# Optimization experiments

Measured on AMD Instinct MI355X. Metric: run time of the kernel, lower is better.

Reference implementation:

```python
import jax, jax.numpy as jnp
import numpy as np

B = 16
N_IN_PER = 256
N_SKIP_PER = 1024
C_IN = 256
C_SKIP = 128


def setup_inputs() -> dict:
    key = jax.random.key(0)
    ks = jax.random.split(key, 8)
    n_in = B * N_IN_PER
    n_skip = B * N_SKIP_PER
    in_x = jax.random.normal(ks[0], (n_in, C_IN), dtype=jnp.float32)
    in_pos = jax.random.uniform(ks[1], (n_in, 3), dtype=jnp.float32)
    in_batch = jnp.repeat(jnp.arange(B, dtype=jnp.int64), N_IN_PER)
    skip_x = jax.random.normal(ks[2], (n_skip, C_SKIP), dtype=jnp.float32)
    skip_pos = jax.random.uniform(ks[3], (n_skip, 3), dtype=jnp.float32)
    skip_batch = jnp.repeat(jnp.arange(B, dtype=jnp.int64), N_SKIP_PER)
    d_cat = C_IN + C_SKIP + 3  # 387
    W1 = jax.random.normal(ks[4], (d_cat, 256), dtype=jnp.float32) * (1.0 / np.sqrt(d_cat))
    b1 = jnp.zeros((256,), dtype=jnp.float32)
    W2 = jax.random.normal(ks[5], (256, 256), dtype=jnp.float32) * (1.0 / 16.0)
    b2 = jnp.zeros((256,), dtype=jnp.float32)
    return {"in_x": in_x, "in_pos": in_pos, "in_batch": in_batch,
            "skip_x": skip_x, "skip_pos": skip_pos, "skip_batch": skip_batch,
            "W1": W1, "b1": b1, "W2": W2, "b2": b2, "knn_num": 3}


def _knn_interpolate(in_x, in_pos, in_batch, skip_pos, skip_batch, k):
    # Pairwise squared distances fine->coarse, masked across graphs. [Ns, Ni]
    d2 = jnp.sum((skip_pos[:, None, :] - in_pos[None, :, :]) ** 2, axis=-1)
    cross = skip_batch[:, None] != in_batch[None, :]
    d2 = jnp.where(cross, jnp.inf, d2)
    _, idx = jax.lax.top_k(-d2, k)  # [Ns, k] nearest coarse neighbors
    nb_pos = in_pos[idx]  # [Ns, k, 3]
    dist = jnp.sqrt(jnp.sum((nb_pos - skip_pos[:, None, :]) ** 2, axis=-1))
    dist = jnp.maximum(dist, 1e-10)
    w = 1.0 / dist
    w = w / (jnp.sum(w, axis=-1, keepdims=True) + 1e-16)  # per-target normalization
    return jnp.einsum('nk,nkc->nc', w, in_x[idx])  # [Ns, C_in]


def reference(in_x, in_pos, in_batch, skip_x, skip_pos, skip_batch, W1, b1, W2, b2, knn_num):
    interp = _knn_interpolate(in_x, in_pos, in_batch, skip_pos, skip_batch, knn_num)
    h = jnp.concatenate([interp, skip_x, skip_pos], axis=1)  # [Ns, 387]
    h = jax.nn.relu(h @ W1 + b1)
    h = jax.nn.relu(h @ W2 + b2)
    return h
```

## Files before the change

kernel.cpp:

```cpp
#include <hip/hip_runtime.h>
#include <hip/hip_bf16.h>


typedef __bf16 bf16x8 __attribute__((ext_vector_type(8)));
typedef float  f32x4  __attribute__((ext_vector_type(4)));

__device__ __forceinline__ unsigned short f2bf(float f) {
  __hip_bfloat16 h = __float2bfloat16(f);
  return __builtin_bit_cast(unsigned short, h);
}

#define GLDS16(G, L)                                                          \
  __builtin_amdgcn_global_load_lds(                                           \
      (const __attribute__((address_space(1))) void*)(G),                     \
      (__attribute__((address_space(3))) void*)(L), 16, 0, 0)

static constexpr int MROWS  = 16384;
static constexpr int KPAD   = 416;
static constexpr int KREAL  = 387;

__global__ __launch_bounds__(256) void prep_weights(
    const float* __restrict__ W1, const float* __restrict__ W2,
    unsigned short* __restrict__ W1t, unsigned short* __restrict__ W2t)
{
  const int k = blockIdx.x;
  const int n = threadIdx.x;
  {
    float v = (k < KREAL) ? W1[(size_t)k * 256 + n] : 0.f;
    W1t[(size_t)n * KPAD + k] = f2bf(v);
  }
  if (k < 256) {
    W2t[(size_t)n * 256 + k] = f2bf(W2[(size_t)k * 256 + n]);
  }
}

__global__ __launch_bounds__(256) void knn_build_h(
    const float* __restrict__ in_x,
    const float* __restrict__ in_pos,
    const float* __restrict__ skip_x,
    const float* __restrict__ skip_pos,
    unsigned short* __restrict__ H)
{
  __shared__ float P[3][256];
  const int tid = threadIdx.x;
  const int s0  = blockIdx.x << 2;
  const int ib  = (s0 >> 10) << 8;
  {
    const float* bp = in_pos + (size_t)ib * 3;
    for (int i = tid; i < 768; i += 256) P[i % 3][i / 3] = bp[i];
  }
  __syncthreads();

  const int wid = tid >> 6, lane = tid & 63;
  const int s = s0 + wid;
  const float sx = skip_pos[(size_t)s * 3 + 0];
  const float sy = skip_pos[(size_t)s * 3 + 1];
  const float sz = skip_pos[(size_t)s * 3 + 2];

  float d2[4];
#pragma unroll
  for (int q = 0; q < 4; ++q) {
    const int i = lane + (q << 6);
    const float dx = __fsub_rn(sx, P[0][i]);
    const float dy = __fsub_rn(sy, P[1][i]);
    const float dz = __fsub_rn(sz, P[2][i]);
    d2[q] = __fadd_rn(__fadd_rn(__fmul_rn(dx, dx), __fmul_rn(dy, dy)),
                      __fmul_rn(dz, dz));
  }

  int   gsel[3];
  float wsel[3];
  float wsum = 0.f;
#pragma unroll
  for (int p = 0; p < 3; ++p) {
    float bd = d2[0];
    int   bi = lane;
#pragma unroll
    for (int q = 1; q < 4; ++q) {
      const int i = lane + (q << 6);
      if (d2[q] < bd) { bd = d2[q]; bi = i; }
    }
#pragma unroll
    for (int m = 1; m < 64; m <<= 1) {
      const float od = __shfl_xor(bd, m);
      const int   oi = __shfl_xor(bi, m);
      if (od < bd || (od == bd && oi < bi)) { bd = od; bi = oi; }
    }
    if ((bi & 63) == lane) d2[bi >> 6] = 3.4e38f;
    gsel[p] = bi;
    const float dx = __fsub_rn(P[0][bi], sx);
    const float dy = __fsub_rn(P[1][bi], sy);
    const float dz = __fsub_rn(P[2][bi], sz);
    float dist = sqrtf(__fadd_rn(__fadd_rn(__fmul_rn(dx, dx), __fmul_rn(dy, dy)),
                                 __fmul_rn(dz, dz)));
    dist = fmaxf(dist, 1e-10f);
    const float w = 1.0f / dist;
    wsel[p] = w;
    wsum += w;
  }
  const float denom = wsum + 1e-16f;
  const float w0 = wsel[0] / denom;
  const float w1 = wsel[1] / denom;
  const float w2 = wsel[2] / denom;

  const f32x4* x0 = (const f32x4*)(in_x + (size_t)(ib + gsel[0]) * 256);
  const f32x4* x1 = (const f32x4*)(in_x + (size_t)(ib + gsel[1]) * 256);
  const f32x4* x2 = (const f32x4*)(in_x + (size_t)(ib + gsel[2]) * 256);
  const f32x4 a = x0[lane], b = x1[lane], c = x2[lane];

  unsigned short* hr = H + (size_t)s * KPAD;
  ushort4 o4;
  o4.x = f2bf(w0 * a.x + w1 * b.x + w2 * c.x);
  o4.y = f2bf(w0 * a.y + w1 * b.y + w2 * c.y);
  o4.z = f2bf(w0 * a.z + w1 * b.z + w2 * c.z);
  o4.w = f2bf(w0 * a.w + w1 * b.w + w2 * c.w);
  *(ushort4*)(hr + (lane << 2)) = o4;

  const float2 sv = ((const float2*)(skip_x + (size_t)s * 128))[lane];
  ushort2 o2;
  o2.x = f2bf(sv.x);
  o2.y = f2bf(sv.y);
  *(ushort2*)(hr + 256 + (lane << 1)) = o2;

  if (lane < 32) {
    float v = (lane == 0) ? sx : (lane == 1) ? sy : (lane == 2) ? sz : 0.f;
    hr[384 + lane] = f2bf(v);
  }
}

template <int K, bool OUT_BF16>
__global__ __launch_bounds__(256) void gemm_bt_relu(
    const unsigned short* __restrict__ A,
    const unsigned short* __restrict__ Bt,
    const float* __restrict__ bias,
    void* __restrict__ Out)
{
  __shared__ unsigned short As[128 * 32];
  __shared__ unsigned short Bs[128 * 32];
  const int tid = threadIdx.x, lane = tid & 63, wid = tid >> 6;
  const int m0 = blockIdx.x << 7, n0 = blockIdx.y << 7;

  const int srow = tid >> 2;
  const int scol = (tid & 3) << 3;
  const unsigned short* gA0 = A + (size_t)(m0 + srow) * K + scol;
  const unsigned short* gA1 = gA0 + (size_t)64 * K;
  const unsigned short* gB0 = Bt + (size_t)(n0 + srow) * K + scol;
  const unsigned short* gB1 = gB0 + (size_t)64 * K;
  unsigned short* lA0 = As + wid * 512;
  unsigned short* lA1 = As + 2048 + wid * 512;
  unsigned short* lB0 = Bs + wid * 512;
  unsigned short* lB1 = Bs + 2048 + wid * 512;

  const int wr = (wid >> 1) << 6;
  const int wc = (wid & 1) << 6;
  const int fr = lane & 15;
  const int ko = (lane >> 4) << 3;

  f32x4 acc[4][4] = {};

  for (int ks = 0; ks < K / 32; ++ks) {
    const int k0 = ks << 5;
    GLDS16(gA0 + k0, lA0);
    GLDS16(gA1 + k0, lA1);
    GLDS16(gB0 + k0, lB0);
    GLDS16(gB1 + k0, lB1);
    __syncthreads();
    bf16x8 af[4], bf[4];
#pragma unroll
    for (int m = 0; m < 4; ++m)
      af[m] = *(const bf16x8*)&As[(wr + m * 16 + fr) * 32 + ko];
#pragma unroll
    for (int n = 0; n < 4; ++n)
      bf[n] = *(const bf16x8*)&Bs[(wc + n * 16 + fr) * 32 + ko];
#pragma unroll
    for (int m = 0; m < 4; ++m)
#pragma unroll
      for (int n = 0; n < 4; ++n)
        acc[m][n] =
            __builtin_amdgcn_mfma_f32_16x16x32_bf16(af[m], bf[n], acc[m][n], 0, 0, 0);
    __syncthreads();
  }

  const int r0 = m0 + wr + ((lane >> 4) << 2);
  const int c0 = n0 + wc + fr;
  float bn[4];
#pragma unroll
  for (int n = 0; n < 4; ++n) bn[n] = bias[c0 + n * 16];
#pragma unroll
  for (int m = 0; m < 4; ++m) {
#pragma unroll
    for (int j = 0; j < 4; ++j) {
      const size_t row = (size_t)(r0 + m * 16 + j);
#pragma unroll
      for (int n = 0; n < 4; ++n) {
        const float v = fmaxf(acc[m][n][j] + bn[n], 0.f);
        if constexpr (OUT_BF16)
          ((unsigned short*)Out)[row * 256 + c0 + n * 16] = f2bf(v);
        else
          ((float*)Out)[row * 256 + c0 + n * 16] = v;
      }
    }
  }
}

extern "C" void kernel_launch(void* const* d_in, const int* in_sizes, int n_in,
                              void* d_out, int out_size, void* d_ws, size_t ws_size,
                              hipStream_t stream) {
  const float* in_x     = (const float*)d_in[0];
  const float* in_pos   = (const float*)d_in[1];
  const float* skip_x   = (const float*)d_in[3];
  const float* skip_pos = (const float*)d_in[4];
  const float* W1       = (const float*)d_in[6];
  const float* bias1    = (const float*)d_in[7];
  const float* W2       = (const float*)d_in[8];
  const float* bias2    = (const float*)d_in[9];

  char* ws = (char*)d_ws;
  unsigned short* H   = (unsigned short*)(ws);
  unsigned short* h1  = (unsigned short*)(ws + 13631488);
  unsigned short* W1t = (unsigned short*)(ws + 13631488 + 8388608);
  unsigned short* W2t = (unsigned short*)(ws + 13631488 + 8388608 + 212992);

  prep_weights<<<dim3(KPAD), dim3(256), 0, stream>>>(W1, W2, W1t, W2t);
  knn_build_h<<<dim3(MROWS / 4), dim3(256), 0, stream>>>(in_x, in_pos, skip_x,
                                                         skip_pos, H);
  gemm_bt_relu<KPAD, true><<<dim3(MROWS / 128, 2), dim3(256), 0, stream>>>(
      H, W1t, bias1, (void*)h1);
  gemm_bt_relu<256, false><<<dim3(MROWS / 128, 2), dim3(256), 0, stream>>>(
      h1, W2t, bias2, d_out);
}
```

Before: 48.58 us.

## Pipeline GEMM loads four-deep with swizzled LDS, tile weight transpose, simplify kNN

Both GEMMs now use a four-buffer LDS ring, keeping three stages of global-to-LDS loads in flight with explicit vmcnt waits. An XOR swizzle on the LDS layout avoids bank conflicts, and the epilogue writes vectorised stores. The weight transpose becomes a tiled shared-memory transpose over 44 blocks with coalesced accesses. The kNN kernel reuses the selected squared distance instead of recomputing it and replaces a dynamically indexed register write with selects. The deeper ring raises LDS use per block, which may lower occupancy.

```diff
diff --git a/kernel.cpp b/kernel.cpp
--- a/kernel.cpp
+++ b/kernel.cpp
@@ -15,26 +15,52 @@
       (const __attribute__((address_space(1))) void*)(G),                     \
       (__attribute__((address_space(3))) void*)(L), 16, 0, 0)
 
-static constexpr int MROWS  = 16384;
-static constexpr int KPAD   = 416;
-static constexpr int KREAL  = 387;
-
-__global__ __launch_bounds__(256) void prep_weights(
+#define BAR()    __builtin_amdgcn_s_barrier()
+#define WAITV(N) asm volatile("s_waitcnt vmcnt(" #N ")" ::: "memory")
+#define WAITL()  asm volatile("s_waitcnt lgkmcnt(0)" ::: "memory")
+
+static constexpr int MROWS = 16384;
+static constexpr int KPAD  = 416;
+static constexpr int KREAL = 387;
+
+__global__ __launch_bounds__(256) void prep_w(
     const float* __restrict__ W1, const float* __restrict__ W2,
     unsigned short* __restrict__ W1t, unsigned short* __restrict__ W2t)
 {
-  const int k = blockIdx.x;
-  const int n = threadIdx.x;
-  {
-    float v = (k < KREAL) ? W1[(size_t)k * 256 + n] : 0.f;
-    W1t[(size_t)n * KPAD + k] = f2bf(v);
-  }
-  if (k < 256) {
-    W2t[(size_t)n * 256 + k] = f2bf(W2[(size_t)k * 256 + n]);
-  }
-}
-
-__global__ __launch_bounds__(256) void knn_build_h(
+  __shared__ float T[64][65];
+  int b = blockIdx.x;
+  const float* S; unsigned short* D; int KP, Kreal, kb, nb;
+  if (b < 28) { S = W1; D = W1t; KP = KPAD; Kreal = KREAL; kb = b >> 2; nb = b & 3; }
+  else { b -= 28; S = W2; D = W2t; KP = 256; Kreal = 256; kb = b >> 2; nb = b & 3; }
+  const int k0 = kb << 6, n0 = nb << 6;
+  const int tr = threadIdx.x >> 4, tc = threadIdx.x & 15;
+#pragma unroll
+  for (int i = 0; i < 4; ++i) {
+    const int k = k0 + i * 16 + tr;
+    float4 v = make_float4(0.f, 0.f, 0.f, 0.f);
+    if (k < Kreal) v = *(const float4*)(S + (size_t)k * 256 + n0 + tc * 4);
+    T[i * 16 + tr][tc * 4 + 0] = v.x;
+    T[i * 16 + tr][tc * 4 + 1] = v.y;
+    T[i * 16 + tr][tc * 4 + 2] = v.z;
+    T[i * 16 + tr][tc * 4 + 3] = v.w;
+  }
+  __syncthreads();
+#pragma unroll
+  for (int i = 0; i < 4; ++i) {
+    const int n = n0 + i * 16 + tr;
+    const int k = k0 + tc * 4;
+    if (k < KP) {
+      ushort4 o;
+      o.x = f2bf(T[tc * 4 + 0][i * 16 + tr]);
+      o.y = f2bf(T[tc * 4 + 1][i * 16 + tr]);
+      o.z = f2bf(T[tc * 4 + 2][i * 16 + tr]);
+      o.w = f2bf(T[tc * 4 + 3][i * 16 + tr]);
+      *(ushort4*)(D + (size_t)n * KP + k) = o;
+    }
+  }
+}
+
+__global__ __launch_bounds__(256) void knn_h(
     const float* __restrict__ in_x,
     const float* __restrict__ in_pos,
     const float* __restrict__ skip_x,
@@ -86,15 +112,14 @@
       const int   oi = __shfl_xor(bi, m);
       if (od < bd || (od == bd && oi < bi)) { bd = od; bi = oi; }
     }
-    if ((bi & 63) == lane) d2[bi >> 6] = 3.4e38f;
+    const bool win = ((bi & 63) == lane);
+    const int  qw  = bi >> 6;
+    d2[0] = (win && qw == 0) ? 3.4e38f : d2[0];
+    d2[1] = (win && qw == 1) ? 3.4e38f : d2[1];
+    d2[2] = (win && qw == 2) ? 3.4e38f : d2[2];
+    d2[3] = (win && qw == 3) ? 3.4e38f : d2[3];
     gsel[p] = bi;
-    const float dx = __fsub_rn(P[0][bi], sx);
-    const float dy = __fsub_rn(P[1][bi], sy);
-    const float dz = __fsub_rn(P[2][bi], sz);
-    float dist = sqrtf(__fadd_rn(__fadd_rn(__fmul_rn(dx, dx), __fmul_rn(dy, dy)),
-                                 __fmul_rn(dz, dz)));
-    dist = fmaxf(dist, 1e-10f);
-    const float w = 1.0f / dist;
+    const float w = 1.0f / fmaxf(sqrtf(bd), 1e-10f);
     wsel[p] = w;
     wsum += w;
   }
@@ -103,10 +128,9 @@
   const float w1 = wsel[1] / denom;
   const float w2 = wsel[2] / denom;
 
-  const f32x4* x0 = (const f32x4*)(in_x + (size_t)(ib + gsel[0]) * 256);
-  const f32x4* x1 = (const f32x4*)(in_x + (size_t)(ib + gsel[1]) * 256);
-  const f32x4* x2 = (const f32x4*)(in_x + (size_t)(ib + gsel[2]) * 256);
-  const f32x4 a = x0[lane], b = x1[lane], c = x2[lane];
+  const f32x4 a = *(const f32x4*)(in_x + (size_t)(ib + gsel[0]) * 256 + lane * 4);
+  const f32x4 b = *(const f32x4*)(in_x + (size_t)(ib + gsel[1]) * 256 + lane * 4);
+  const f32x4 c = *(const f32x4*)(in_x + (size_t)(ib + gsel[2]) * 256 + lane * 4);
 
   unsigned short* hr = H + (size_t)s * KPAD;
   ushort4 o4;
@@ -128,76 +152,97 @@
   }
 }
 
-template <int K, bool OUT_BF16>
-__global__ __launch_bounds__(256) void gemm_bt_relu(
+template <int K, int NK, bool OUT_BF16>
+__global__ __launch_bounds__(256) void gemm_p3(
     const unsigned short* __restrict__ A,
     const unsigned short* __restrict__ Bt,
     const float* __restrict__ bias,
     void* __restrict__ Out)
 {
-  __shared__ unsigned short As[128 * 32];
-  __shared__ unsigned short Bs[128 * 32];
+  __shared__ unsigned short As[4][128 * 32];
+  __shared__ unsigned short Bs[4][128 * 32];
   const int tid = threadIdx.x, lane = tid & 63, wid = tid >> 6;
   const int m0 = blockIdx.x << 7, n0 = blockIdx.y << 7;
-
-  const int srow = tid >> 2;
-  const int scol = (tid & 3) << 3;
-  const unsigned short* gA0 = A + (size_t)(m0 + srow) * K + scol;
+  const int fr = lane & 15, g = lane >> 4;
+  const int wr = (wid >> 1) << 6, wcc = (wid & 1) << 6;
+
+  const int r  = tid >> 2;
+  const int cs = (tid & 3) ^ ((r >> 1) & 3);
+  const unsigned short* gA0 = A + (size_t)(m0 + r) * K + cs * 8;
   const unsigned short* gA1 = gA0 + (size_t)64 * K;
-  const unsigned short* gB0 = Bt + (size_t)(n0 + srow) * K + scol;
+  const unsigned short* gB0 = Bt + (size_t)(n0 + r) * K + cs * 8;
   const unsigned short* gB1 = gB0 + (size_t)64 * K;
-  unsigned short* lA0 = As + wid * 512;
-  unsigned short* lA1 = As + 2048 + wid * 512;
-  unsigned short* lB0 = Bs + wid * 512;
-  unsigned short* lB1 = Bs + 2048 + wid * 512;
-
-  const int wr = (wid >> 1) << 6;
-  const int wc = (wid & 1) << 6;
-  const int fr = lane & 15;
-  const int ko = (lane >> 4) << 3;
+
+#define STAGE(ks, b)                                                          \
+  {                                                                           \
+    const int _ko = (ks) * 32;                                                \
+    GLDS16(gA0 + _ko, &As[b][wid * 512]);                                     \
+    GLDS16(gA1 + _ko, &As[b][2048 + wid * 512]);                              \
+    GLDS16(gB0 + _ko, &Bs[b][wid * 512]);                                     \
+    GLDS16(gB1 + _ko, &Bs[b][2048 + wid * 512]);                              \
+  }
+
+  int woff[4], hoff[4];
+#pragma unroll
+  for (int i = 0; i < 4; ++i) {
+    const int Rw = wcc + i * 16 + fr;
+    const int Rh = wr + i * 16 + fr;
+    woff[i] = Rw * 32 + ((g ^ ((Rw >> 1) & 3)) << 3);
+    hoff[i] = Rh * 32 + ((g ^ ((Rh >> 1) & 3)) << 3);
+  }
+
+  STAGE(0, 0); STAGE(1, 1); STAGE(2, 2);
 
   f32x4 acc[4][4] = {};
 
-  for (int ks = 0; ks < K / 32; ++ks) {
-    const int k0 = ks << 5;
-    GLDS16(gA0 + k0, lA0);
-    GLDS16(gA1 + k0, lA1);
-    GLDS16(gB0 + k0, lB0);
-    GLDS16(gB1 + k0, lB1);
-    __syncthreads();
-    bf16x8 af[4], bf[4];
-#pragma unroll
-    for (int m = 0; m < 4; ++m)
-      af[m] = *(const bf16x8*)&As[(wr + m * 16 + fr) * 32 + ko];
-#pragma unroll
-    for (int n = 0; n < 4; ++n)
-      bf[n] = *(const bf16x8*)&Bs[(wc + n * 16 + fr) * 32 + ko];
-#pragma unroll
-    for (int m = 0; m < 4; ++m)
-#pragma unroll
-      for (int n = 0; n < 4; ++n)
-        acc[m][n] =
-            __builtin_amdgcn_mfma_f32_16x16x32_bf16(af[m], bf[n], acc[m][n], 0, 0, 0);
-    __syncthreads();
-  }
-
-  const int r0 = m0 + wr + ((lane >> 4) << 2);
-  const int c0 = n0 + wc + fr;
-  float bn[4];
-#pragma unroll
-  for (int n = 0; n < 4; ++n) bn[n] = bias[c0 + n * 16];
-#pragma unroll
-  for (int m = 0; m < 4; ++m) {
-#pragma unroll
-    for (int j = 0; j < 4; ++j) {
-      const size_t row = (size_t)(r0 + m * 16 + j);
-#pragma unroll
-      for (int n = 0; n < 4; ++n) {
-        const float v = fmaxf(acc[m][n][j] + bn[n], 0.f);
-        if constexpr (OUT_BF16)
-          ((unsigned short*)Out)[row * 256 + c0 + n * 16] = f2bf(v);
-        else
-          ((float*)Out)[row * 256 + c0 + n * 16] = v;
+#pragma unroll 1
+  for (int ks = 0; ks < NK; ++ks) {
+    if (ks + 3 < NK) STAGE(ks + 3, (ks + 3) & 3);
+    const int rem = NK - 1 - ks;
+    if (rem >= 3)      { WAITV(12); }
+    else if (rem == 2) { WAITV(8); }
+    else if (rem == 1) { WAITV(4); }
+    else               { WAITV(0); }
+    BAR();
+    const unsigned short* as = As[ks & 3];
+    const unsigned short* bs = Bs[ks & 3];
+    bf16x8 wf[4], hf[4];
+#pragma unroll
+    for (int i = 0; i < 4; ++i) wf[i] = *(const bf16x8*)&bs[woff[i]];
+#pragma unroll
+    for (int i = 0; i < 4; ++i) hf[i] = *(const bf16x8*)&as[hoff[i]];
+#pragma unroll
+    for (int mc = 0; mc < 4; ++mc)
+#pragma unroll
+      for (int rr = 0; rr < 4; ++rr)
+        acc[mc][rr] = __builtin_amdgcn_mfma_f32_16x16x32_bf16(
+            wf[mc], hf[rr], acc[mc][rr], 0, 0, 0);
+    WAITL(); BAR();
+  }
+#undef STAGE
+
+  f32x4 bv[4];
+#pragma unroll
+  for (int mc = 0; mc < 4; ++mc)
+    bv[mc] = *(const f32x4*)(bias + n0 + wcc + mc * 16 + g * 4);
+#pragma unroll
+  for (int rr = 0; rr < 4; ++rr) {
+    const size_t row = (size_t)(m0 + wr + rr * 16 + fr);
+#pragma unroll
+    for (int mc = 0; mc < 4; ++mc) {
+      const int col = n0 + wcc + mc * 16 + g * 4;
+      if constexpr (OUT_BF16) {
+        ushort4 o;
+        o.x = f2bf(fmaxf(acc[mc][rr][0] + bv[mc][0], 0.f));
+        o.y = f2bf(fmaxf(acc[mc][rr][1] + bv[mc][1], 0.f));
+        o.z = f2bf(fmaxf(acc[mc][rr][2] + bv[mc][2], 0.f));
+        o.w = f2bf(fmaxf(acc[mc][rr][3] + bv[mc][3], 0.f));
+        *(ushort4*)((unsigned short*)Out + row * 256 + col) = o;
+      } else {
+        f32x4 o;
+#pragma unroll
+        for (int j = 0; j < 4; ++j) o[j] = fmaxf(acc[mc][rr][j] + bv[mc][j], 0.f);
+        *(f32x4*)((float*)Out + row * 256 + col) = o;
       }
     }
   }
@@ -216,16 +261,16 @@
   const float* bias2    = (const float*)d_in[9];
 
   char* ws = (char*)d_ws;
-  unsigned short* H   = (unsigned short*)(ws);
-  unsigned short* h1  = (unsigned short*)(ws + 13631488);
-  unsigned short* W1t = (unsigned short*)(ws + 13631488 + 8388608);
-  unsigned short* W2t = (unsigned short*)(ws + 13631488 + 8388608 + 212992);
-
-  prep_weights<<<dim3(KPAD), dim3(256), 0, stream>>>(W1, W2, W1t, W2t);
-  knn_build_h<<<dim3(MROWS / 4), dim3(256), 0, stream>>>(in_x, in_pos, skip_x,
-                                                         skip_pos, H);
-  gemm_bt_relu<KPAD, true><<<dim3(MROWS / 128, 2), dim3(256), 0, stream>>>(
+  unsigned short* W1t = (unsigned short*)(ws);
+  unsigned short* W2t = (unsigned short*)(ws + 212992);
+  unsigned short* H   = (unsigned short*)(ws + 212992 + 131072);
+  unsigned short* h1  = (unsigned short*)(ws + 212992 + 131072 + 13631488);
+
+  prep_w<<<dim3(44), dim3(256), 0, stream>>>(W1, W2, W1t, W2t);
+  knn_h<<<dim3(MROWS / 4), dim3(256), 0, stream>>>(in_x, in_pos, skip_x,
+                                                   skip_pos, H);
+  gemm_p3<KPAD, 13, true><<<dim3(MROWS / 128, 2), dim3(256), 0, stream>>>(
       H, W1t, bias1, (void*)h1);
-  gemm_bt_relu<256, false><<<dim3(MROWS / 128, 2), dim3(256), 0, stream>>>(
+  gemm_p3<256, 8, false><<<dim3(MROWS / 128, 2), dim3(256), 0, stream>>>(
       h1, W2t, bias2, d_out);
 }
```

After: 47.48 us. 1.02x faster.
